# Kernel optimization log

Hardware: AMD Instinct MI355X
Metric: run time of the kernel (lower is better)

Reference implementation:

```python
import jax, jax.numpy as jnp
import numpy as np

NEG_SLOPE = 0.2   # LeakyReLU default negative slope (GATv2 + nn.LeakyReLU)
K_NEIGH = 16      # att_args['num_neighs']


def leaky(x):
    return jnp.where(x >= 0, x, NEG_SLOPE * x)


def knn_idx(x_feat, y_feat, k):
    """Per-batch KNN of y in x (feature space). x_feat,y_feat: [B,M,C] -> [B,M,k] local idx into x."""
    d = (jnp.sum(y_feat * y_feat, -1, keepdims=True)
         - 2.0 * jnp.einsum('bmc,bnc->bmn', y_feat, x_feat)
         + jnp.sum(x_feat * x_feat, -1)[:, None, :])   # [B,M,M]
    _, idx = jax.lax.top_k(-d, k)
    return idx


def gatv2_bipartite(x_last, x_past, nbr, Wl, Wr, att_w):
    """Faithful GATv2Conv((last, past), edge_index) with flow='target_to_source',
    heads H, concat=False (mean over heads), bias=False, no self loops.
    x_j = lin_l(x[0]=last) gathered at knn neighbor (col) indices,
    x_i = lin_r(x[1]=past) at query (row) indices; each query has exactly K edges."""
    N, C = x_last.shape
    H = att_w.shape[0]
    xl = (x_last @ Wl).reshape(N, H, C)          # [N,H,C]
    xr = (x_past @ Wr).reshape(N, H, C)          # [N,H,C]
    xlj = xl[nbr]                                 # [N,K,H,C] gathered source msgs
    e = jnp.einsum('nkhc,hc->nkh', leaky(xlj + xr[:, None]), att_w)  # [N,K,H]
    a = jax.nn.softmax(e, axis=1)                 # softmax over each target's K edges
    out = jnp.einsum('nkh,nkhc->nhc', a, xlj)     # [N,H,C]
    return out.mean(axis=1)                       # concat=False -> head mean, [N,C]


def reference(pc_encoded_seq, W1, b1, W2, b2, Wl, Wr, att_w, batch_size, m_points):
    T, N, C = pc_encoded_seq.shape
    B, M = batch_size, m_points
    G = W2.shape[1]
    # node_level_proj (Linear-LeakyReLU-Linear-LeakyReLU) + global_mean_pool per frame
    h = leaky(leaky(pc_encoded_seq @ W1 + b1) @ W2 + b2)      # [T,N,G]
    global_fea = h.reshape(T, B, M, G).mean(axis=2)            # [T,B,G]
    # frame-level ScaledDotProductAttention: q = last frame, k=v = past frames
    q = global_fea[-1][:, None, :]                             # [B,1,G]
    kv = jnp.transpose(global_fea[:-1], (1, 0, 2))             # [B,T-1,G]
    score = jnp.einsum('bqg,btg->bqt', q, kv) / jnp.sqrt(jnp.asarray(G, jnp.float32))
    attn = jax.nn.softmax(score, axis=-1)                      # [B,1,T-1]
    last = pc_encoded_seq[-1]                                  # [N,C]
    lastb = last.reshape(B, M, C)
    offs = (jnp.arange(B) * M)[:, None, None]
    res = []
    for i in range(T - 1):   # small fixed frame count
        past = pc_encoded_seq[i]
        nbr = knn_idx(past.reshape(B, M, C), lastb, K_NEIGH) + offs  # global idx
        out = gatv2_bipartite(last, past, nbr.reshape(N, K_NEIGH), Wl, Wr, att_w)
        res.append(out.reshape(B, M, C))
    res = jnp.stack(res, axis=1)                               # [B,T-1,M,C]
    fw = attn[:, 0, :, None, None]                             # [B,T-1,1,1]
    weighted = jnp.sum(res * fw, axis=1)                       # [B,M,C]
    tm_out = jnp.concatenate([last, weighted.reshape(N, C)], axis=-1)  # [N,2C]
    return tm_out


def setup_inputs() -> dict:
    key = jax.random.key(0)
    ks = jax.random.split(key, 8)
    T, B, M, C, G, H = 5, 4, 4096, 128, 1024, 4
    N = B * M
    s = lambda fan: 1.0 / np.sqrt(fan)
    return {
        'pc_encoded_seq': jax.random.normal(ks[0], (T, N, C), jnp.float32),
        'W1': jax.random.normal(ks[1], (C, 128), jnp.float32) * s(C),
        'b1': jnp.zeros((128,), jnp.float32),
        'W2': jax.random.normal(ks[2], (128, G), jnp.float32) * s(128),
        'b2': jnp.zeros((G,), jnp.float32),
        'Wl': jax.random.normal(ks[3], (C, H * C), jnp.float32) * s(C),
        'Wr': jax.random.normal(ks[4], (C, H * C), jnp.float32) * s(C),
        'att_w': jax.random.normal(ks[5], (H, C), jnp.float32) * s(C),
        'batch_size': B,
        'm_points': M,
    }
```

## Files before the change

### kernel.cpp

```cpp
#include <hip/hip_runtime.h>
#include <hip/hip_bf16.h>
#include <hip/hip_fp16.h>


typedef __bf16 v8bf __attribute__((ext_vector_type(8)));
typedef float  v4f  __attribute__((ext_vector_type(4)));

__device__ __forceinline__ float lrelu(float x) { return fmaxf(x, 0.2f * x); }

__device__ __forceinline__ unsigned short f2bf(float x) {
  __hip_bfloat16 h = __float2bfloat16(x);
  return __builtin_bit_cast(unsigned short, h);
}
__device__ __forceinline__ float bf2f(unsigned short u) {
  unsigned int t = ((unsigned int)u) << 16;
  return __builtin_bit_cast(float, t);
}

#define GLOAD_LDS16(gp, lp)                                                   \
  __builtin_amdgcn_global_load_lds(                                           \
      (const __attribute__((address_space(1))) void*)(gp),                    \
      (__attribute__((address_space(3))) void*)(lp), 16, 0, 0)

#define RBAR() do { __builtin_amdgcn_s_barrier(); asm volatile("" ::: "memory"); } while (0)
#define LWAIT() do { asm volatile("s_waitcnt lgkmcnt(0)" ::: "memory");        \
                     __builtin_amdgcn_sched_barrier(0); } while (0)

template<int EP>
__global__ __launch_bounds__(256, 2)
void nt_mfma(const unsigned short* __restrict__ A, const unsigned short* __restrict__ B,
             const float* __restrict__ aux, void* __restrict__ outv, int K, int ldc)
{
  __shared__ __align__(16) unsigned short smem[3 * 8192];
  const int tid = threadIdx.x;
  const int l = tid & 63;
  const int w = tid >> 6;
  const int wm = w & 1, wn = w >> 1;
  const int m0 = blockIdx.y << 7, n0 = blockIdx.x << 7;
  const int fr = l & 15, quad = l >> 4;
  const int kt = K >> 5;
  const int xq4 = quad ^ ((fr >> 1) & 3);

  const int r0 = tid >> 2;
  const int sw = (tid & 3) ^ ((tid >> 3) & 3);
  const unsigned short* Aa = A + (size_t)(m0 + r0) * K + sw * 8;
  const unsigned short* Ab = Aa + (size_t)64 * K;
  const unsigned short* Ba = B + (size_t)(n0 + r0) * K + sw * 8;
  const unsigned short* Bb = Ba + (size_t)64 * K;

  auto stage = [&](int bi, int ks) {
    unsigned short* As = smem + bi * 8192;
    unsigned short* Bs = As + 4096;
    GLOAD_LDS16(Aa + ks * 32, As + tid * 8);
    GLOAD_LDS16(Ab + ks * 32, As + (tid + 256) * 8);
    GLOAD_LDS16(Ba + ks * 32, Bs + tid * 8);
    GLOAD_LDS16(Bb + ks * 32, Bs + (tid + 256) * 8);
  };

  v4f acc[4][4];
#pragma unroll
  for (int i = 0; i < 4; ++i)
#pragma unroll
    for (int j = 0; j < 4; ++j) acc[i][j] = (v4f){0.f, 0.f, 0.f, 0.f};

  stage(0, 0);
  if (kt > 1) stage(1, 1);
  int cur = 0, pend = (kt > 1) ? 2 : 1, sn = 2;

  for (int ks = 0; ks < kt; ++ks) {
    if (pend == 2) asm volatile("s_waitcnt vmcnt(4)" ::: "memory");
    else           asm volatile("s_waitcnt vmcnt(0)" ::: "memory");
    RBAR();
    int nb = cur + 2; if (nb >= 3) nb -= 3;
    if (sn < kt) { stage(nb, sn); ++sn; } else { --pend; }
    const unsigned short* As = smem + cur * 8192;
    const unsigned short* Bs = As + 4096;
    v8bf af[4], bfr[4];
#pragma unroll
    for (int i = 0; i < 4; ++i)
      af[i] = *(const v8bf*)(As + (wm * 64 + i * 16 + fr) * 32 + xq4 * 8);
#pragma unroll
    for (int j = 0; j < 4; ++j)
      bfr[j] = *(const v8bf*)(Bs + (wn * 64 + j * 16 + fr) * 32 + xq4 * 8);
#pragma unroll
    for (int i = 0; i < 4; ++i)
#pragma unroll
      for (int j = 0; j < 4; ++j)
        acc[i][j] = __builtin_amdgcn_mfma_f32_16x16x32_bf16(af[i], bfr[j], acc[i][j], 0, 0, 0);
    __builtin_amdgcn_sched_barrier(0);
    if (++cur == 3) cur = 0;
  }

  if (EP == 1) {
    unsigned short* O = (unsigned short*)outv;
#pragma unroll
    for (int j = 0; j < 4; ++j) {
      int col = n0 + wn * 64 + j * 16 + fr;
      float bias = aux[col];
#pragma unroll
      for (int i = 0; i < 4; ++i) {
        int row = m0 + wm * 64 + i * 16 + quad * 4;
#pragma unroll
        for (int r = 0; r < 4; ++r)
          O[(size_t)(row + r) * ldc + col] = f2bf(lrelu(acc[i][j][r] + bias));
      }
    }
  } else if (EP == 2) {
    __syncthreads();
    float* red = (float*)smem;
#pragma unroll
    for (int j = 0; j < 4; ++j) {
      int lcol = wn * 64 + j * 16 + fr;
      float bias = aux[n0 + lcol];
      float s = 0.f;
#pragma unroll
      for (int i = 0; i < 4; ++i)
#pragma unroll
        for (int r = 0; r < 4; ++r) s += lrelu(acc[i][j][r] + bias);
      s += __shfl_xor(s, 16);
      s += __shfl_xor(s, 32);
      if (quad == 0) red[w * 128 + lcol] = s;
    }
    __syncthreads();
    if (tid < 128) {
      float s = (tid < 64) ? red[0 * 128 + tid] + red[1 * 128 + tid]
                           : red[2 * 128 + tid] + red[3 * 128 + tid];
      atomicAdd((float*)outv + ((m0 >> 12) << 10) + n0 + tid, s * (1.0f / 4096.0f));
    }
  } else {
    __half* O = (__half*)outv;
#pragma unroll
    for (int j = 0; j < 4; ++j) {
      int col = n0 + wn * 64 + j * 16 + fr;
#pragma unroll
      for (int i = 0; i < 4; ++i) {
        int row = m0 + wm * 64 + i * 16 + quad * 4;
#pragma unroll
        for (int r = 0; r < 4; ++r)
          O[(size_t)(row + r) * ldc + col] = __float2half(acc[i][j][r]);
      }
    }
  }
}

#define TOPN 24
#define TSTR 25
#define FB   16
#define PSTR 17

__global__ __launch_bounds__(256, 2)
void knn_coarse(const unsigned short* __restrict__ seqbf,
                const float* __restrict__ xsq, int* __restrict__ candOut)
{
  __shared__ __align__(16) unsigned short smem[16384];
  __shared__ float topV[128 * TSTR];
  __shared__ int   topI[128 * TSTR];
  __shared__ float pushV[128 * PSTR];
  __shared__ int   pushI[128 * PSTR];
  __shared__ int   cntW[128];

  const int tid = threadIdx.x;
  const int l = tid & 63;
  const int w = tid >> 6;
  const int pair = blockIdx.x >> 5;
  const int rb = blockIdx.x & 31;
  const int f = pair >> 2, b = pair & 3;
  const int m0 = rb << 7;
  const int fr = l & 15, quad = l >> 4;
  const int xq4 = quad ^ ((fr >> 1) & 3);

  const unsigned short* ybase = seqbf + ((size_t)65536 + b * 4096) * 128;
  const unsigned short* xbase = seqbf + ((size_t)(f * 16384 + b * 4096)) * 128;
  const float* xq = xsq + f * 16384 + b * 4096;

  const int r0 = tid >> 2;
  const int sw = (tid & 3) ^ ((tid >> 3) & 3);

#pragma unroll
  for (int kk = 0; kk < 4; ++kk) {
    const unsigned short* Ag = ybase + (size_t)(m0 + r0) * 128 + kk * 32 + sw * 8;
    GLOAD_LDS16(Ag, smem + kk * 4096 + tid * 8);
    GLOAD_LDS16(Ag + 64 * 128, smem + kk * 4096 + (tid + 256) * 8);
  }
  asm volatile("s_waitcnt vmcnt(0)" ::: "memory");
  RBAR();

  v8bf afr[4][2];
#pragma unroll
  for (int kk = 0; kk < 4; ++kk)
#pragma unroll
    for (int i = 0; i < 2; ++i)
      afr[kk][i] = *(const v8bf*)(smem + kk * 4096 + (w * 32 + i * 16 + fr) * 32 + xq4 * 8);
  LWAIT();

  float tauReg = -3.0e38f;
  float ownMin = -3.0e38f;
  int   ownMinPos = 0;
  if (l < 32) {
    const int grow = w * 32 + l;
#pragma unroll
    for (int k = 0; k < TOPN; ++k) { topV[grow * TSTR + k] = -3.0e38f; topI[grow * TSTR + k] = k; }
    cntW[grow] = 0;
  }
  float tc[8];
#pragma unroll
  for (int i = 0; i < 8; ++i) tc[i] = -3.0e38f;

  for (int ct = 0; ct < 32; ++ct) {
    const int n0 = ct << 7;
    RBAR();
    {
      const unsigned short* Bt = xbase + (size_t)(n0 + r0) * 128 + sw * 8;
#pragma unroll
      for (int kk = 0; kk < 4; ++kk) {
        GLOAD_LDS16(Bt + kk * 32, smem + kk * 4096 + tid * 8);
        GLOAD_LDS16(Bt + 64 * 128 + kk * 32, smem + kk * 4096 + (tid + 256) * 8);
      }
    }
    float xsv[8];
#pragma unroll
    for (int j = 0; j < 8; ++j) xsv[j] = xq[n0 + j * 16 + fr];
    asm volatile("s_waitcnt vmcnt(0)" ::: "memory");
    RBAR();

    v4f acc[2][8];
#pragma unroll
    for (int i = 0; i < 2; ++i)
#pragma unroll
      for (int j = 0; j < 8; ++j) acc[i][j] = (v4f){0.f, 0.f, 0.f, 0.f};

#pragma unroll
    for (int ksp = 0; ksp < 4; ++ksp) {
      v8bf bfr[8];
#pragma unroll
      for (int j = 0; j < 8; ++j)
        bfr[j] = *(const v8bf*)(smem + ksp * 4096 + (j * 16 + fr) * 32 + xq4 * 8);
#pragma unroll
      for (int i = 0; i < 2; ++i)
#pragma unroll
        for (int j = 0; j < 8; ++j)
          acc[i][j] = __builtin_amdgcn_mfma_f32_16x16x32_bf16(afr[ksp][i], bfr[j], acc[i][j], 0, 0, 0);
    }

    unsigned long long pushed = 0ull;
    for (;;) {
#pragma unroll
      for (int i = 0; i < 2; ++i)
#pragma unroll
        for (int r = 0; r < 4; ++r) {
          const int grow = w * 32 + i * 16 + quad * 4 + r;
          const float tau = tc[i * 4 + r];
#pragma unroll
          for (int j = 0; j < 8; ++j) {
            const int bit = i * 32 + j * 4 + r;
            float v = 2.f * acc[i][j][r] - xsv[j];
            if (v > tau && !((pushed >> bit) & 1ull)) {
              int pos = atomicAdd(&cntW[grow], 1);
              if (pos < FB) {
                pushV[grow * PSTR + pos] = v;
                pushI[grow * PSTR + pos] = n0 + j * 16 + fr;
                pushed |= (1ull << bit);
              }
            }
          }
        }
      LWAIT();
      bool ov = false;
      if (l < 32) {
        const int grow = w * 32 + l;
        int c = cntW[grow];
        int cc = c < FB ? c : FB;
        for (int q = 0; q < cc; ++q) {
          float v = pushV[grow * PSTR + q];
          if (v > ownMin) {
            topV[grow * TSTR + ownMinPos] = v;
            topI[grow * TSTR + ownMinPos] = pushI[grow * PSTR + q];
            ownMin = topV[grow * TSTR];
            ownMinPos = 0;
#pragma unroll
            for (int k = 1; k < TOPN; ++k) {
              float tk = topV[grow * TSTR + k];
              if (tk < ownMin) { ownMin = tk; ownMinPos = k; }
            }
          }
        }
        tauReg = ownMin;
        ov = c > FB;
        cntW[grow] = 0;
      }
      LWAIT();
#pragma unroll
      for (int i = 0; i < 2; ++i)
#pragma unroll
        for (int r = 0; r < 4; ++r)
          tc[i * 4 + r] = __shfl(tauReg, i * 16 + quad * 4 + r);
      if (!__any(ov)) break;
    }
  }

  if (l < 32) {
    const int grow = w * 32 + l;
    int* outp = candOut + ((size_t)(f * 16384 + b * 4096 + m0 + grow)) * TOPN;
#pragma unroll
    for (int k = 0; k < TOPN; ++k) outp[k] = topI[grow * TSTR + k];
  }
}

__global__ __launch_bounds__(256)
void knn_rescore(const float* __restrict__ seq, const float* __restrict__ xsq,
                 const int* __restrict__ cand, int* __restrict__ nbrOut)
{
  const int tid = threadIdx.x;
  const int l = tid & 63;
  const int gq = blockIdx.x * 4 + (tid >> 6);
  const int f = gq >> 14;
  const int rem = gq & 16383;
  const int b = rem >> 12;
  const float2 yv = ((const float2*)(seq + ((size_t)65536 + rem) * 128))[l];
  const float* xslice = seq + (size_t)(f * 16384 + (b << 12)) * 128;
  const float* xsqs = xsq + f * 16384 + (b << 12);

  const int myi = cand[(size_t)gq * 24 + (l < 24 ? l : 0)];
  const float xsq_mine = xsqs[myi];

  float2 xv[24];
#pragma unroll
  for (int j = 0; j < 24; ++j) {
    int cj = __shfl(myi, j);
    xv[j] = ((const float2*)(xslice + (size_t)cj * 128))[l];
  }
  float p[24];
#pragma unroll
  for (int j = 0; j < 24; ++j) p[j] = yv.x * xv[j].x + yv.y * xv[j].y;
#pragma unroll
  for (int off = 1; off <= 32; off <<= 1)
#pragma unroll
    for (int j = 0; j < 24; ++j) p[j] += __shfl_xor(p[j], off);

  float myv = -3.0e38f;
#pragma unroll
  for (int j = 0; j < 24; ++j) if (l == j) myv = 2.f * p[j] - xsq_mine;

  int rank = 0;
#pragma unroll
  for (int j = 0; j < 24; ++j) {
    float vj = __shfl(myv, j);
    rank += (vj > myv || (vj == myv && j < l)) ? 1 : 0;
  }
  if (l < 24 && rank < 16)
    nbrOut[(size_t)gq * 16 + rank] = (b << 12) + myi;
}

__global__ __launch_bounds__(256)
void convert_inputs(const float* __restrict__ seq, unsigned short* __restrict__ seqbf,
                    unsigned short* __restrict__ ylay, unsigned short* __restrict__ xlay,
                    float* __restrict__ xsq)
{
  const int tid = threadIdx.x;
  const int row = blockIdx.x * 8 + (tid >> 5);
  const int c4 = tid & 31;
  float4 v = *(const float4*)(seq + (size_t)row * 128 + c4 * 4);
  ushort4 hi, lo;
  hi.x = f2bf(v.x); lo.x = f2bf(v.x - bf2f(hi.x));
  hi.y = f2bf(v.y); lo.y = f2bf(v.y - bf2f(hi.y));
  hi.z = f2bf(v.z); lo.z = f2bf(v.z - bf2f(hi.z));
  hi.w = f2bf(v.w); lo.w = f2bf(v.w - bf2f(hi.w));
  *(ushort4*)(seqbf + (size_t)row * 128 + c4 * 4) = hi;
  float ss = v.x * v.x + v.y * v.y + v.z * v.z + v.w * v.w;
#pragma unroll
  for (int off = 16; off; off >>= 1) ss += __shfl_xor(ss, off);
  if (row < 65536) {
    unsigned short* p = xlay + (size_t)row * 384 + c4 * 4;
    *(ushort4*)(p) = hi; *(ushort4*)(p + 128) = lo; *(ushort4*)(p + 256) = hi;
    if (c4 == 0) xsq[row] = ss;
  } else {
    unsigned short* p = ylay + (size_t)(row - 65536) * 384 + c4 * 4;
    *(ushort4*)(p) = hi; *(ushort4*)(p + 128) = hi; *(ushort4*)(p + 256) = lo;
  }
}

__global__ __launch_bounds__(256)
void convert_weights(const float* __restrict__ W1, const float* __restrict__ W2,
                     const float* __restrict__ Wl, const float* __restrict__ Wr,
                     const float* __restrict__ aw,
                     unsigned short* __restrict__ W1t, unsigned short* __restrict__ W2t,
                     unsigned short* __restrict__ Wlv, unsigned short* __restrict__ Wrv,
                     __half* __restrict__ awh)
{
  int idx = blockIdx.x * 256 + threadIdx.x;
  if (idx < 16384) {
    int n = idx >> 7, k = idx & 127;
    W1t[idx] = f2bf(W1[k * 128 + n]);
  } else if (idx < 147456) {
    int i = idx - 16384; int n = i >> 7, k = i & 127;
    W2t[i] = f2bf(W2[k * 1024 + n]);
  } else if (idx < 344064) {
    int i = idx - 147456; int n = i / 384, k = i % 384;
    int s = k >> 7, kk = k & 127;
    float wv = Wl[kk * 512 + n];
    unsigned short h = f2bf(wv);
    Wlv[i] = (s == 1) ? f2bf(wv - bf2f(h)) : h;
  } else if (idx < 540672) {
    int i = idx - 344064; int n = i / 384, k = i % 384;
    int s = k >> 7, kk = k & 127;
    float wv = Wr[kk * 512 + n];
    unsigned short h = f2bf(wv);
    Wrv[i] = (s == 2) ? f2bf(wv - bf2f(h)) : h;
  } else if (idx < 541184) {
    int i = idx - 540672;
    awh[i] = __float2half(aw[i]);
  }
}

__global__ __launch_bounds__(1024)
void temporal_attn(const float* __restrict__ gfea, float* __restrict__ attnw)
{
  const int tid = threadIdx.x;
  const int w = tid >> 6, l = tid & 63;
  const int b = w >> 2, i = w & 3;
  const float* q  = gfea + (16 + b) * 1024;
  const float* kv = gfea + (i * 4 + b) * 1024;
  float p = 0.f;
  for (int g = l; g < 1024; g += 64) p += q[g] * kv[g];
#pragma unroll
  for (int off = 32; off; off >>= 1) p += __shfl_xor(p, off);
  __shared__ float sc[16];
  if (l == 0) sc[w] = p * 0.03125f;
  __syncthreads();
  if (tid < 4) {
    float v0 = sc[tid * 4 + 0], v1 = sc[tid * 4 + 1];
    float v2 = sc[tid * 4 + 2], v3 = sc[tid * 4 + 3];
    float mm = fmaxf(fmaxf(v0, v1), fmaxf(v2, v3));
    v0 = __expf(v0 - mm); v1 = __expf(v1 - mm);
    v2 = __expf(v2 - mm); v3 = __expf(v3 - mm);
    float inv = 1.f / (v0 + v1 + v2 + v3);
    attnw[tid * 4 + 0] = v0 * inv;
    attnw[tid * 4 + 1] = v1 * inv;
    attnw[tid * 4 + 2] = v2 * inv;
    attnw[tid * 4 + 3] = v3 * inv;
  }
}

__global__ __launch_bounds__(256)
void gat6(const __half* __restrict__ xlh, const __half* __restrict__ xrh,
          const int* __restrict__ nbr, const __half* __restrict__ awh,
          const float* __restrict__ attnw, float* __restrict__ wgt4)
{
  const int tid = threadIdx.x;
  const int l = tid & 63;
  const int blk = blockIdx.x;
  const int r8 = blk & 7;
  const int b = r8 >> 1;
  const int g = ((blk >> 3) << 1) | (r8 & 1);
  const int f = g >> 10;
  const int n4 = g & 1023;
  const int qid = f * 16384 + b * 4096 + n4 * 4 + (tid >> 6);
  const int h = l >> 4, cp = l & 15;
  const float fw = attnw[b * 4 + f] * 0.25f;

  const int jl = nbr[qid * 16 + (l & 15)];
  const __half* xbase = xlh + h * 128 + cp * 8;

  const __half2* xrp = (const __half2*)(xrh + (size_t)qid * 512 + h * 128 + cp * 8);
  float2 xr0 = __half22float2(xrp[0]), xr1 = __half22float2(xrp[1]);
  float2 xr2 = __half22float2(xrp[2]), xr3 = __half22float2(xrp[3]);
  const __half2* awp = (const __half2*)(awh + h * 128 + cp * 8);
  float2 aw0 = __half22float2(awp[0]), aw1 = __half22float2(awp[1]);
  float2 aw2 = __half22float2(awp[2]), aw3 = __half22float2(awp[3]);

  float m = -3.0e38f, s = 0.f;
  float o[8];
#pragma unroll
  for (int c = 0; c < 8; ++c) o[c] = 0.f;

  for (int ch = 0; ch < 2; ++ch) {
    float4 xv[8];
#pragma unroll
    for (int k = 0; k < 8; ++k) {
      int j = __shfl(jl, ch * 8 + k);
      xv[k] = *(const float4*)(xbase + (size_t)j * 512);
    }
    float e[8];
#pragma unroll
    for (int k = 0; k < 8; ++k) {
      const __half2* hp = (const __half2*)&xv[k];
      float2 x0 = __half22float2(hp[0]), x1 = __half22float2(hp[1]);
      float2 x2 = __half22float2(hp[2]), x3 = __half22float2(hp[3]);
      float p = 0.f;
      p += lrelu(x0.x + xr0.x) * aw0.x + lrelu(x0.y + xr0.y) * aw0.y;
      p += lrelu(x1.x + xr1.x) * aw1.x + lrelu(x1.y + xr1.y) * aw1.y;
      p += lrelu(x2.x + xr2.x) * aw2.x + lrelu(x2.y + xr2.y) * aw2.y;
      p += lrelu(x3.x + xr3.x) * aw3.x + lrelu(x3.y + xr3.y) * aw3.y;
      p += __shfl_xor(p, 1);
      p += __shfl_xor(p, 2);
      p += __shfl_xor(p, 4);
      p += __shfl_xor(p, 8);
      e[k] = p;
    }
    float mc = e[0];
#pragma unroll
    for (int k = 1; k < 8; ++k) mc = fmaxf(mc, e[k]);
    float mn = fmaxf(m, mc);
    float cr = __expf(m - mn);
    s *= cr;
#pragma unroll
    for (int c = 0; c < 8; ++c) o[c] *= cr;
#pragma unroll
    for (int k = 0; k < 8; ++k) {
      float a = __expf(e[k] - mn);
      s += a;
      const __half2* hp = (const __half2*)&xv[k];
      float2 f0 = __half22float2(hp[0]);
      float2 f1 = __half22float2(hp[1]);
      float2 f2 = __half22float2(hp[2]);
      float2 f3 = __half22float2(hp[3]);
      o[0] += a * f0.x; o[1] += a * f0.y;
      o[2] += a * f1.x; o[3] += a * f1.y;
      o[4] += a * f2.x; o[5] += a * f2.y;
      o[6] += a * f3.x; o[7] += a * f3.y;
    }
    m = mn;
  }

  const float sc = fw / s;
#pragma unroll
  for (int c = 0; c < 8; ++c) {
    float t = o[c] * sc;
    t += __shfl_xor(t, 16);
    t += __shfl_xor(t, 32);
    o[c] = t;
  }
  if (l < 16) {
    float* wp = wgt4 + (size_t)qid * 128 + l * 8;
    *(float4*)(wp)     = make_float4(o[0], o[1], o[2], o[3]);
    *(float4*)(wp + 4) = make_float4(o[4], o[5], o[6], o[7]);
  }
}

__global__ __launch_bounds__(256)
void finalize2(const float* __restrict__ last, const float* __restrict__ wgt4,
               float* __restrict__ out)
{
  int idx = blockIdx.x * 256 + threadIdx.x;
  int n = idx >> 6, q = idx & 63;
  float4 v;
  if (q < 32) {
    v = *(const float4*)(last + (size_t)n * 128 + 4 * q);
  } else {
    int c = (q - 32) * 4;
    v = make_float4(0.f, 0.f, 0.f, 0.f);
#pragma unroll
    for (int f = 0; f < 4; ++f) {
      float4 t = *(const float4*)(wgt4 + ((size_t)f * 16384 + n) * 128 + c);
      v.x += t.x; v.y += t.y; v.z += t.z; v.w += t.w;
    }
  }
  *(float4*)(out + (size_t)n * 256 + 4 * q) = v;
}

extern "C" void kernel_launch(void* const* d_in, const int* in_sizes, int n_in,
                              void* d_out, int out_size, void* d_ws, size_t ws_size,
                              hipStream_t stream)
{
  (void)in_sizes; (void)n_in; (void)out_size; (void)ws_size;
  const float* seq = (const float*)d_in[0];
  const float* W1  = (const float*)d_in[1];
  const float* b1  = (const float*)d_in[2];
  const float* W2  = (const float*)d_in[3];
  const float* b2  = (const float*)d_in[4];
  const float* Wl  = (const float*)d_in[5];
  const float* Wr  = (const float*)d_in[6];
  const float* aw  = (const float*)d_in[7];
  float* out = (float*)d_out;

  float* ws = (float*)d_ws;
  __half* xrh          = (__half*)ws;
  unsigned short* seqbf = (unsigned short*)(ws + 16777216);
  unsigned short* h1bf  = (unsigned short*)(ws + 22020096);
  int* cand24           = (int*)(ws + 22020096);
  __half* xlh           = (__half*)(ws + 22020096);
  unsigned short* ylay  = (unsigned short*)(ws + 27262976);
  unsigned short* xlay  = (unsigned short*)(ws + 30408704);
  float* wgt4           = ws + 30408704;
  float* gfea           = ws + 42991616;
  float* attn           = gfea + 20480;
  float* xsq            = attn + 16;
  int*   nbr            = (int*)(xsq + 65536);
  unsigned short* W1t   = (unsigned short*)(nbr + 1048576);
  unsigned short* W2t   = W1t + 16384;
  unsigned short* Wlv   = W2t + 131072;
  unsigned short* Wrv   = Wlv + 196608;
  __half* awh           = (__half*)(Wrv + 196608);

  (void)hipMemsetAsync(gfea, 0, 20480 * sizeof(float), stream);

  convert_inputs<<<10240, 256, 0, stream>>>(seq, seqbf, ylay, xlay, xsq);
  convert_weights<<<2114, 256, 0, stream>>>(W1, W2, Wl, Wr, aw, W1t, W2t, Wlv, Wrv, awh);

  nt_mfma<1><<<dim3(1, 640), 256, 0, stream>>>(seqbf, W1t, b1, h1bf, 128, 128);
  nt_mfma<2><<<dim3(8, 640), 256, 0, stream>>>(h1bf, W2t, b2, gfea, 128, 0);
  temporal_attn<<<1, 1024, 0, stream>>>(gfea, attn);

  knn_coarse<<<512, 256, 0, stream>>>(seqbf, xsq, cand24);
  knn_rescore<<<16384, 256, 0, stream>>>(seq, xsq, cand24, nbr);

  nt_mfma<3><<<dim3(4, 128), 256, 0, stream>>>(ylay, Wlv, nullptr, xlh, 384, 512);
  nt_mfma<3><<<dim3(4, 512), 256, 0, stream>>>(xlay, Wrv, nullptr, xrh, 384, 512);

  gat6<<<16384, 256, 0, stream>>>(xlh, xrh, nbr, awh, attn, wgt4);

  finalize2<<<4096, 256, 0, stream>>>(seq + (size_t)4 * 16384 * 128, wgt4, out);
}
```

Before: 884.5 us.

## Restructure KNN coarse kernel into single-wave blocks with register-prefetched B tiles

```diff
diff --git a/kernel.cpp b/kernel.cpp
--- a/kernel.cpp
+++ b/kernel.cpp
@@ -148,98 +148,131 @@
 #define FB   16
 #define PSTR 17
 
-__global__ __launch_bounds__(256, 2)
+__global__ __launch_bounds__(64, 2)
 void knn_coarse(const unsigned short* __restrict__ seqbf,
                 const float* __restrict__ xsq, int* __restrict__ candOut)
 {
-  __shared__ __align__(16) unsigned short smem[16384];
-  __shared__ float topV[128 * TSTR];
-  __shared__ int   topI[128 * TSTR];
-  __shared__ float pushV[128 * PSTR];
-  __shared__ int   pushI[128 * PSTR];
-  __shared__ int   cntW[128];
-
-  const int tid = threadIdx.x;
-  const int l = tid & 63;
-  const int w = tid >> 6;
-  const int pair = blockIdx.x >> 5;
-  const int rb = blockIdx.x & 31;
+  __shared__ float topV[32 * TSTR];
+  __shared__ int   topI[32 * TSTR];
+  __shared__ float pushV[32 * PSTR];
+  __shared__ int   pushI[32 * PSTR];
+  __shared__ int   cntW[32];
+
+  const int l = threadIdx.x;
+  const int fr = l & 15, quad = l >> 4;
+  const int blk = blockIdx.x;
+  const int pair = ((blk & 7) << 1) | ((blk >> 3) & 1);
+  const int rb = blk >> 4;
   const int f = pair >> 2, b = pair & 3;
-  const int m0 = rb << 7;
-  const int fr = l & 15, quad = l >> 4;
-  const int xq4 = quad ^ ((fr >> 1) & 3);
+  const int m0 = rb << 5;
 
   const unsigned short* ybase = seqbf + ((size_t)65536 + b * 4096) * 128;
   const unsigned short* xbase = seqbf + ((size_t)(f * 16384 + b * 4096)) * 128;
   const float* xq = xsq + f * 16384 + b * 4096;
-
-  const int r0 = tid >> 2;
-  const int sw = (tid & 3) ^ ((tid >> 3) & 3);
-
-#pragma unroll
-  for (int kk = 0; kk < 4; ++kk) {
-    const unsigned short* Ag = ybase + (size_t)(m0 + r0) * 128 + kk * 32 + sw * 8;
-    GLOAD_LDS16(Ag, smem + kk * 4096 + tid * 8);
-    GLOAD_LDS16(Ag + 64 * 128, smem + kk * 4096 + (tid + 256) * 8);
-  }
-  asm volatile("s_waitcnt vmcnt(0)" ::: "memory");
-  RBAR();
+  const unsigned short* bb = xbase + fr * 128 + quad * 8;
 
   v8bf afr[4][2];
 #pragma unroll
-  for (int kk = 0; kk < 4; ++kk)
+  for (int ksp = 0; ksp < 4; ++ksp)
 #pragma unroll
     for (int i = 0; i < 2; ++i)
-      afr[kk][i] = *(const v8bf*)(smem + kk * 4096 + (w * 32 + i * 16 + fr) * 32 + xq4 * 8);
-  LWAIT();
-
+      afr[ksp][i] = *(const v8bf*)(ybase + (size_t)(m0 + i * 16 + fr) * 128 + ksp * 32 + quad * 8);
+
+  if (l < 32) {
+#pragma unroll
+    for (int k = 0; k < TOPN; ++k) { topV[l * TSTR + k] = -3.0e38f; topI[l * TSTR + k] = k; }
+    cntW[l] = 0;
+  }
   float tauReg = -3.0e38f;
   float ownMin = -3.0e38f;
   int   ownMinPos = 0;
-  if (l < 32) {
-    const int grow = w * 32 + l;
-#pragma unroll
-    for (int k = 0; k < TOPN; ++k) { topV[grow * TSTR + k] = -3.0e38f; topI[grow * TSTR + k] = k; }
-    cntW[grow] = 0;
-  }
   float tc[8];
 #pragma unroll
   for (int i = 0; i < 8; ++i) tc[i] = -3.0e38f;
+
+  v8bf bf[16];
+  float xsv[8], xsp[8];
+#pragma unroll
+  for (int j = 0; j < 8; ++j) bf[j]     = *(const v8bf*)(bb + (size_t)j * 2048);
+#pragma unroll
+  for (int j = 0; j < 8; ++j) bf[8 + j] = *(const v8bf*)(bb + (size_t)j * 2048 + 32);
+#pragma unroll
+  for (int j = 0; j < 8; ++j) xsv[j] = xq[j * 16 + fr];
+
+  v4f acc[2][8];
 
   for (int ct = 0; ct < 32; ++ct) {
     const int n0 = ct << 7;
-    RBAR();
-    {
-      const unsigned short* Bt = xbase + (size_t)(n0 + r0) * 128 + sw * 8;
-#pragma unroll
-      for (int kk = 0; kk < 4; ++kk) {
-        GLOAD_LDS16(Bt + kk * 32, smem + kk * 4096 + tid * 8);
-        GLOAD_LDS16(Bt + 64 * 128 + kk * 32, smem + kk * 4096 + (tid + 256) * 8);
-      }
-    }
-    float xsv[8];
-#pragma unroll
-    for (int j = 0; j < 8; ++j) xsv[j] = xq[n0 + j * 16 + fr];
-    asm volatile("s_waitcnt vmcnt(0)" ::: "memory");
-    RBAR();
-
-    v4f acc[2][8];
+    const unsigned short* bp = bb + (size_t)n0 * 128;
+
 #pragma unroll
     for (int i = 0; i < 2; ++i)
 #pragma unroll
       for (int j = 0; j < 8; ++j) acc[i][j] = (v4f){0.f, 0.f, 0.f, 0.f};
 
 #pragma unroll
-    for (int ksp = 0; ksp < 4; ++ksp) {
-      v8bf bfr[8];
-#pragma unroll
-      for (int j = 0; j < 8; ++j)
-        bfr[j] = *(const v8bf*)(smem + ksp * 4096 + (j * 16 + fr) * 32 + xq4 * 8);
+    for (int j = 0; j < 8; ++j)
 #pragma unroll
       for (int i = 0; i < 2; ++i)
-#pragma unroll
-        for (int j = 0; j < 8; ++j)
-          acc[i][j] = __builtin_amdgcn_mfma_f32_16x16x32_bf16(afr[ksp][i], bfr[j], acc[i][j], 0, 0, 0);
+        acc[i][j] = __builtin_amdgcn_mfma_f32_16x16x32_bf16(afr[0][i], bf[j], acc[i][j], 0, 0, 0);
+#pragma unroll
+    for (int j = 0; j < 8; ++j) bf[j] = *(const v8bf*)(bp + (size_t)j * 2048 + 64);
+#pragma unroll
+    for (int j = 0; j < 8; ++j)
+#pragma unroll
+      for (int i = 0; i < 2; ++i)
+        acc[i][j] = __builtin_amdgcn_mfma_f32_16x16x32_bf16(afr[1][i], bf[8 + j], acc[i][j], 0, 0, 0);
+#pragma unroll
+    for (int j = 0; j < 8; ++j) bf[8 + j] = *(const v8bf*)(bp + (size_t)j * 2048 + 96);
+
+#pragma unroll
+    for (int j = 0; j < 8; ++j) xsp[j] = xsv[j];
+    if (ct < 31) {
+#pragma unroll
+      for (int j = 0; j < 8; ++j) xsv[j] = xq[((ct + 1) << 7) + j * 16 + fr];
+    }
+
+#pragma unroll
+    for (int j = 0; j < 8; ++j)
+#pragma unroll
+      for (int i = 0; i < 2; ++i)
+        acc[i][j] = __builtin_amdgcn_mfma_f32_16x16x32_bf16(afr[2][i], bf[j], acc[i][j], 0, 0, 0);
+#pragma unroll
+    for (int j = 0; j < 8; ++j)
+#pragma unroll
+      for (int i = 0; i < 2; ++i)
+        acc[i][j] = __builtin_amdgcn_mfma_f32_16x16x32_bf16(afr[3][i], bf[8 + j], acc[i][j], 0, 0, 0);
+
+    if (ct < 31) {
+      const unsigned short* bn = bb + (size_t)((ct + 1) << 7) * 128;
+#pragma unroll
+      for (int j = 0; j < 8; ++j) bf[j]     = *(const v8bf*)(bn + (size_t)j * 2048);
+#pragma unroll
+      for (int j = 0; j < 8; ++j) bf[8 + j] = *(const v8bf*)(bn + (size_t)j * 2048 + 32);
+    }
+
+    if (ct == 0) {
+#pragma unroll
+      for (int i = 0; i < 2; ++i)
+#pragma unroll
+        for (int r = 0; r < 4; ++r) {
+          float v0 = 2.f * acc[i][0][r] - xsp[0];
+          float v1 = 2.f * acc[i][1][r] - xsp[1];
+          float t1 = fmaxf(v0, v1), t2 = fminf(v0, v1);
+#pragma unroll
+          for (int j = 2; j < 8; ++j) {
+            float v = 2.f * acc[i][j][r] - xsp[j];
+            float hi = fmaxf(t1, v);
+            t2 = fmaxf(t2, fminf(t1, v));
+            t1 = hi;
+          }
+#pragma unroll
+          for (int off = 1; off <= 8; off <<= 1)
+            t2 = fminf(t2, __shfl_xor(t2, off));
+          tc[i * 4 + r] = t2;
+          float tq = __shfl(t2, ((l >> 2) & 3) << 4);
+          if (l < 32 && (l >> 4) == i && (l & 3) == r) tauReg = tq;
+        }
     }
 
     unsigned long long pushed = 0ull;
@@ -248,45 +281,50 @@
       for (int i = 0; i < 2; ++i)
 #pragma unroll
         for (int r = 0; r < 4; ++r) {
-          const int grow = w * 32 + i * 16 + quad * 4 + r;
           const float tau = tc[i * 4 + r];
+          int m = 0;
 #pragma unroll
           for (int j = 0; j < 8; ++j) {
+            float v = 2.f * acc[i][j][r] - xsp[j];
             const int bit = i * 32 + j * 4 + r;
-            float v = 2.f * acc[i][j][r] - xsv[j];
-            if (v > tau && !((pushed >> bit) & 1ull)) {
-              int pos = atomicAdd(&cntW[grow], 1);
-              if (pos < FB) {
-                pushV[grow * PSTR + pos] = v;
-                pushI[grow * PSTR + pos] = n0 + j * 16 + fr;
-                pushed |= (1ull << bit);
+            if (v > tau && !((pushed >> bit) & 1ull)) m |= (1 << j);
+          }
+          unsigned long long bal = __ballot(m != 0);
+          if ((bal >> (quad << 4)) & 0xFFFFull) {
+            const int lrow = i * 16 + quad * 4 + r;
+#pragma unroll
+            for (int j = 0; j < 8; ++j)
+              if ((m >> j) & 1) {
+                int pos = atomicAdd(&cntW[lrow], 1);
+                if (pos < FB) {
+                  pushV[lrow * PSTR + pos] = 2.f * acc[i][j][r] - xsp[j];
+                  pushI[lrow * PSTR + pos] = n0 + j * 16 + fr;
+                  pushed |= (1ull << (i * 32 + j * 4 + r));
+                }
               }
-            }
           }
         }
       LWAIT();
       bool ov = false;
       if (l < 32) {
-        const int grow = w * 32 + l;
-        int c = cntW[grow];
+        int c = cntW[l];
         int cc = c < FB ? c : FB;
         for (int q = 0; q < cc; ++q) {
-          float v = pushV[grow * PSTR + q];
+          float v = pushV[l * PSTR + q];
           if (v > ownMin) {
-            topV[grow * TSTR + ownMinPos] = v;
-            topI[grow * TSTR + ownMinPos] = pushI[grow * PSTR + q];
-            ownMin = topV[grow * TSTR];
-            ownMinPos = 0;
+            topV[l * TSTR + ownMinPos] = v;
+            topI[l * TSTR + ownMinPos] = pushI[l * PSTR + q];
+            ownMin = topV[l * TSTR]; ownMinPos = 0;
 #pragma unroll
             for (int k = 1; k < TOPN; ++k) {
-              float tk = topV[grow * TSTR + k];
+              float tk = topV[l * TSTR + k];
               if (tk < ownMin) { ownMin = tk; ownMinPos = k; }
             }
           }
         }
-        tauReg = ownMin;
+        tauReg = fmaxf(tauReg, ownMin);
         ov = c > FB;
-        cntW[grow] = 0;
+        cntW[l] = 0;
       }
       LWAIT();
 #pragma unroll
@@ -299,10 +337,9 @@
   }
 
   if (l < 32) {
-    const int grow = w * 32 + l;
-    int* outp = candOut + ((size_t)(f * 16384 + b * 4096 + m0 + grow)) * TOPN;
-#pragma unroll
-    for (int k = 0; k < TOPN; ++k) outp[k] = topI[grow * TSTR + k];
+    int* outp = candOut + ((size_t)(f * 16384 + b * 4096 + m0 + l)) * TOPN;
+#pragma unroll
+    for (int k = 0; k < TOPN; ++k) outp[k] = topI[l * TSTR + k];
   }
 }
 
@@ -312,11 +349,14 @@
 {
   const int tid = threadIdx.x;
   const int l = tid & 63;
-  const int gq = blockIdx.x * 4 + (tid >> 6);
-  const int f = gq >> 14;
-  const int rem = gq & 16383;
-  const int b = rem >> 12;
-  const float2 yv = ((const float2*)(seq + ((size_t)65536 + rem) * 128))[l];
+  const int blk = blockIdx.x;
+  const int pair = ((blk & 7) << 1) | ((blk >> 3) & 1);
+  const int qb = blk >> 4;
+  const int f = pair >> 2, b = pair & 3;
+  const int qloc = qb * 4 + (tid >> 6);
+  const int gq = pair * 4096 + qloc;
+
+  const float2 yv = ((const float2*)(seq + ((size_t)65536 + b * 4096 + qloc) * 128))[l];
   const float* xslice = seq + (size_t)(f * 16384 + (b << 12)) * 128;
   const float* xsqs = xsq + f * 16384 + (b << 12);
 
@@ -601,7 +641,7 @@
   nt_mfma<2><<<dim3(8, 640), 256, 0, stream>>>(h1bf, W2t, b2, gfea, 128, 0);
   temporal_attn<<<1, 1024, 0, stream>>>(gfea, attn);
 
-  knn_coarse<<<512, 256, 0, stream>>>(seqbf, xsq, cand24);
+  knn_coarse<<<2048, 64, 0, stream>>>(seqbf, xsq, cand24);
   knn_rescore<<<16384, 256, 0, stream>>>(seq, xsq, cand24, nbr);
 
   nt_mfma<3><<<dim3(4, 128), 256, 0, stream>>>(ylay, Wlv, nullptr, xlh, 384, 512);
```

Measured after the change: 1.013 ms. 14.5% more time.

## Seed KNN threshold from first tile, ballot-gate candidate pushes, remap rescore blocks

Applied to the files above, without the earlier changes.

```diff
diff --git a/kernel.cpp b/kernel.cpp
--- a/kernel.cpp
+++ b/kernel.cpp
@@ -242,26 +242,63 @@
           acc[i][j] = __builtin_amdgcn_mfma_f32_16x16x32_bf16(afr[ksp][i], bfr[j], acc[i][j], 0, 0, 0);
     }
 
+#pragma unroll
+    for (int i = 0; i < 2; ++i)
+#pragma unroll
+      for (int j = 0; j < 8; ++j)
+#pragma unroll
+        for (int r = 0; r < 4; ++r)
+          acc[i][j][r] = 2.f * acc[i][j][r] - xsv[j];
+
+    if (ct == 0) {
+#pragma unroll
+      for (int i = 0; i < 2; ++i)
+#pragma unroll
+        for (int r = 0; r < 4; ++r) {
+          float t1 = fmaxf(acc[i][0][r], acc[i][1][r]);
+          float t2 = fminf(acc[i][0][r], acc[i][1][r]);
+#pragma unroll
+          for (int j = 2; j < 8; ++j) {
+            float v = acc[i][j][r];
+            float hi = fmaxf(t1, v);
+            t2 = fmaxf(t2, fminf(t1, v));
+            t1 = hi;
+          }
+#pragma unroll
+          for (int off = 1; off <= 8; off <<= 1)
+            t2 = fminf(t2, __shfl_xor(t2, off));
+          tc[i * 4 + r] = t2;
+          float tq = __shfl(t2, (((l >> 2) & 3) << 4));
+          if (l < 32 && (l >> 4) == i && (l & 3) == r) tauReg = tq;
+        }
+    }
+
     unsigned long long pushed = 0ull;
     for (;;) {
 #pragma unroll
       for (int i = 0; i < 2; ++i)
 #pragma unroll
         for (int r = 0; r < 4; ++r) {
-          const int grow = w * 32 + i * 16 + quad * 4 + r;
           const float tau = tc[i * 4 + r];
+          int mca = 0;
 #pragma unroll
           for (int j = 0; j < 8; ++j) {
             const int bit = i * 32 + j * 4 + r;
-            float v = 2.f * acc[i][j][r] - xsv[j];
-            if (v > tau && !((pushed >> bit) & 1ull)) {
-              int pos = atomicAdd(&cntW[grow], 1);
-              if (pos < FB) {
-                pushV[grow * PSTR + pos] = v;
-                pushI[grow * PSTR + pos] = n0 + j * 16 + fr;
-                pushed |= (1ull << bit);
+            if (acc[i][j][r] > tau && !((pushed >> bit) & 1ull)) mca |= (1 << j);
+          }
+          unsigned long long bal = __ballot(mca != 0);
+          if ((bal >> (quad << 4)) & 0xFFFFull) {
+            const int lrow = w * 32 + i * 16 + quad * 4 + r;
+#pragma unroll
+            for (int j = 0; j < 8; ++j)
+              if ((mca >> j) & 1) {
+                int pos = atomicAdd(&cntW[lrow], 1);
+                if (pos < FB) {
+                  pushV[lrow * PSTR + pos] = acc[i][j][r];
+                  pushI[lrow * PSTR + pos] = n0 + j * 16 + fr;
+                  pushed |= (1ull << (i * 32 + j * 4 + r));
+                }
               }
-            }
           }
         }
       LWAIT();
@@ -275,8 +312,7 @@
           if (v > ownMin) {
             topV[grow * TSTR + ownMinPos] = v;
             topI[grow * TSTR + ownMinPos] = pushI[grow * PSTR + q];
-            ownMin = topV[grow * TSTR];
-            ownMinPos = 0;
+            ownMin = topV[grow * TSTR]; ownMinPos = 0;
 #pragma unroll
             for (int k = 1; k < TOPN; ++k) {
               float tk = topV[grow * TSTR + k];
@@ -284,7 +320,7 @@
             }
           }
         }
-        tauReg = ownMin;
+        tauReg = fmaxf(tauReg, ownMin);
         ov = c > FB;
         cntW[grow] = 0;
       }
@@ -312,11 +348,14 @@
 {
   const int tid = threadIdx.x;
   const int l = tid & 63;
-  const int gq = blockIdx.x * 4 + (tid >> 6);
-  const int f = gq >> 14;
-  const int rem = gq & 16383;
-  const int b = rem >> 12;
-  const float2 yv = ((const float2*)(seq + ((size_t)65536 + rem) * 128))[l];
+  const int blk = blockIdx.x;
+  const int pair = ((blk & 7) << 1) | ((blk >> 3) & 1);
+  const int qb = blk >> 4;
+  const int f = pair >> 2, b = pair & 3;
+  const int qloc = qb * 4 + (tid >> 6);
+  const int gq = pair * 4096 + qloc;
+
+  const float2 yv = ((const float2*)(seq + ((size_t)65536 + b * 4096 + qloc) * 128))[l];
   const float* xslice = seq + (size_t)(f * 16384 + (b << 12)) * 128;
   const float* xsqs = xsq + f * 16384 + (b << 12);
 
```

Result: slower. 916.4 us (+3.6%).
